# Performance work log

Measured on AMD Instinct MI355X. Metric: run time of the kernel, lower is better.

Reference implementation:

```python
import jax, jax.numpy as jnp
import numpy as np

S = 64    # shapelets_size
N = 256   # num_shapelets
C = 3     # in_channels
B = 64
L = 2048


def setup_inputs() -> dict:
    key = jax.random.key(0)
    kx, ks = jax.random.split(key)
    x = jax.random.normal(kx, (B, C, L), dtype=jnp.float32)
    shapelets = jax.random.normal(ks, (C, N, S), dtype=jnp.float32)
    return {"x": x, "shapelets": shapelets}


def reference(x, shapelets):
    # x: (B, C, L); shapelets: (C, N, S)
    W = x.shape[2] - S + 1  # number of sliding windows
    # unfold: (B, C, W, S)
    idx = jnp.arange(W)[:, None] + jnp.arange(S)[None, :]
    win = x[:, :, idx]
    # cdist with mm-based euclidean: d^2 = |a|^2 + |b|^2 - 2 a.b
    win_sq = jnp.sum(win * win, axis=-1)                 # (B, C, W)
    shp_sq = jnp.sum(shapelets * shapelets, axis=-1)     # (C, N)
    cross = jnp.einsum('bcws,cns->bcwn', win, shapelets)  # (B, C, W, N)
    d2 = win_sq[..., None] + shp_sq[None, :, None, :] - 2.0 * cross
    d = jnp.sqrt(jnp.maximum(d2, 0.0))                   # (B, C, W, N)
    # sum over channels, keepdim -> (B, 1, W, N); transpose -> (B, 1, N, W); min over W
    summed = jnp.sum(d, axis=1, keepdims=True)
    out = jnp.min(jnp.swapaxes(summed, 2, 3), axis=3)    # (B, 1, N)
    return out
```

## Files before the change

### kernel.cpp

```cpp
#include <hip/hip_runtime.h>
#include <hip/hip_fp16.h>


typedef float  v4f __attribute__((ext_vector_type(4)));
typedef short  v8s __attribute__((ext_vector_type(8)));
typedef unsigned short u16;
typedef unsigned int   u32;
typedef unsigned long long u64;

#define S_ 64
#define N_ 256
#define C_ 3
#define B_ 64
#define L_ 2048
#define W_ 1985
#define WQL 512
#define NC 146
#define CSTRIDE 160
#define THREADS 512

__device__ __forceinline__ u16 f2bf(float f) {
    u32 u = __builtin_bit_cast(u32, f);
    return (u16)((u + 0x7FFFu + ((u >> 16) & 1u)) >> 16);
}
__device__ __forceinline__ float bf2f(u16 b) {
    return __builtin_bit_cast(float, ((u32)b) << 16);
}

__global__ __launch_bounds__(THREADS, 4)
void shapelet_min_kernel(const float* __restrict__ x,
                         const float* __restrict__ shp,
                         float* __restrict__ out)
{
    __shared__ u64   xls[C_ * 4 * CSTRIDE];
    __shared__ float wsq[C_][WQL];
    __shared__ u16   scratch[C_ * 64 * 72];
    __shared__ float red[8][64];

    const int tid  = threadIdx.x;
    const int wave = tid >> 6;
    const int lane = tid & 63;
    const int m    = lane & 15;
    const int q    = lane >> 4;
    const int ww   = wave & 3;
    const int wn   = wave >> 2;
    const int blk  = blockIdx.x;
    const int wq   = blk & 3;
    const int nh   = (blk >> 2) & 1;
    const int b    = blk >> 3;
    const int w0   = wq << 9;
    const int wlen = min(WQL, W_ - w0);

    const float* xb = x + (size_t)b * (C_ * L_);
    float xf[8];
    int xc = 0, xt = 0;
    bool xact = (tid < C_ * NC);
    if (xact) {
        xc = tid / NC;
        xt = tid - xc * NC;
        int e = w0 + (xt << 2);
        if (e + 7 < L_) {
            v4f a0 = *(const v4f*)(xb + xc * L_ + e);
            v4f a1 = *(const v4f*)(xb + xc * L_ + e + 4);
            xf[0] = a0[0]; xf[1] = a0[1]; xf[2] = a0[2]; xf[3] = a0[3];
            xf[4] = a1[0]; xf[5] = a1[1]; xf[6] = a1[2]; xf[7] = a1[3];
        } else {
            #pragma unroll
            for (int i = 0; i < 8; ++i)
                xf[i] = (e + i < L_) ? xb[xc * L_ + e + i] : 0.f;
        }
    }

    const int nbase = nh << 7;
    #pragma unroll
    for (int k = 0; k < 6; ++k) {
        int idx = tid + k * THREADS;
        int sq = idx & 15;
        int n  = (idx >> 4) & 63;
        int c  = idx >> 10;
        v4f v = *(const v4f*)(shp + ((size_t)(c * N_ + nbase + n) * S_ + (sq << 2)));
        u64 pk = (u64)f2bf(v[0]) | ((u64)f2bf(v[1]) << 16)
               | ((u64)f2bf(v[2]) << 32) | ((u64)f2bf(v[3]) << 48);
        *(u64*)(scratch + ((c * 64 + n) * 72 + (sq << 2))) = pk;
    }

    if (xact) {
        u16 w8[8];
        #pragma unroll
        for (int i = 0; i < 8; ++i) w8[i] = f2bf(-2.f * xf[i]);
        #pragma unroll
        for (int r = 0; r < 4; ++r) {
            u64 pk = (u64)w8[r] | ((u64)w8[r + 1] << 16)
                   | ((u64)w8[r + 2] << 32) | ((u64)w8[r + 3] << 48);
            xls[(xc * 4 + r) * CSTRIDE + 4 * r + xt] = pk;
        }
    }
    __syncthreads();

    if (tid < 128 * C_) {
        int c  = tid >> 7;
        int t0 = tid & 127;
        const u64* cp0 = &xls[(c * 4) * CSTRIDE];
        u64 ch = cp0[t0];
        float h0 = bf2f((u16)ch),         h1 = bf2f((u16)(ch >> 16)),
              h2 = bf2f((u16)(ch >> 32)), h3 = bf2f((u16)(ch >> 48));
        float sq0 = h0 * h0, sq1 = h1 * h1, sq2 = h2 * h2;
        float s = sq0 + sq1 + sq2 + h3 * h3;
        #pragma unroll
        for (int kk = 1; kk < 16; ++kk) {
            u64 c2 = cp0[t0 + kk];
            float e0 = bf2f((u16)c2),         e1 = bf2f((u16)(c2 >> 16)),
                  e2 = bf2f((u16)(c2 >> 32)), e3 = bf2f((u16)(c2 >> 48));
            s += e0 * e0; s += e1 * e1; s += e2 * e2; s += e3 * e3;
        }
        u64 ct = cp0[t0 + 16];
        float t4 = bf2f((u16)ct), t5 = bf2f((u16)(ct >> 16)), t6 = bf2f((u16)(ct >> 32));
        float s0 = s;
        float s1 = s0 - sq0 + t4 * t4;
        float s2 = s1 - sq1 + t5 * t5;
        float s3 = s2 - sq2 + t6 * t6;
        v4f o = (v4f){0.25f * s0, 0.25f * s1, 0.25f * s2, 0.25f * s3};
        *(v4f*)&wsq[c][t0 << 2] = o;
    }

    const int r  = m & 3;
    const int sE = m >> 2;

    #pragma unroll 1
    for (int g = 0; g < 2; ++g) {
        v8s bfr[C_][2][2];
        float ssq[C_][2];
        #pragma unroll
        for (int c = 0; c < C_; ++c) {
            #pragma unroll
            for (int nt = 0; nt < 2; ++nt) {
                float sacc = 0.f;
                #pragma unroll
                for (int h = 0; h < 2; ++h) {
                    v8s f = *(const v8s*)(scratch +
                             ((c * 64 + wn * 32 + nt * 16 + m) * 72 + h * 32 + q * 8));
                    bfr[c][nt][h] = f;
                    #pragma unroll
                    for (int j = 0; j < 8; ++j) {
                        float e = bf2f((u16)f[j]);
                        sacc += e * e;
                    }
                }
                sacc += __shfl_xor(sacc, 16);
                sacc += __shfl_xor(sacc, 32);
                ssq[c][nt] = sacc;
            }
        }
        __syncthreads();

        float minv[2] = {1e30f, 1e30f};
        #pragma unroll 1
        for (int it = 0; it < 8; ++it) {
            const int wb = it * 64 + ww * 16;
            if (wb >= wlen) continue;

            float sums[2][4];
            #pragma unroll
            for (int nt = 0; nt < 2; ++nt)
                #pragma unroll
                for (int gi = 0; gi < 4; ++gi) sums[nt][gi] = 0.f;

            #pragma unroll
            for (int c = 0; c < C_; ++c) {
                const u64* cp = &xls[(c * 4 + r) * CSTRIDE + 4 * r];
                int T0 = (wb >> 2) + 2 * q + sE;
                union { u64 u[2]; v8s v; } a0, a1;
                a0.u[0] = cp[T0];     a0.u[1] = cp[T0 + 1];
                a1.u[0] = cp[T0 + 8]; a1.u[1] = cp[T0 + 9];

                v4f wv = *(const v4f*)&wsq[c][wb + (q << 2)];
                v4f acc[2];
                #pragma unroll
                for (int nt = 0; nt < 2; ++nt)
                    #pragma unroll
                    for (int gi = 0; gi < 4; ++gi)
                        acc[nt][gi] = wv[gi] + ssq[c][nt];
                #pragma unroll
                for (int nt = 0; nt < 2; ++nt) {
                    acc[nt] = __builtin_amdgcn_mfma_f32_16x16x32_bf16(a0.v, bfr[c][nt][0], acc[nt], 0, 0, 0);
                    acc[nt] = __builtin_amdgcn_mfma_f32_16x16x32_bf16(a1.v, bfr[c][nt][1], acc[nt], 0, 0, 0);
                }
                #pragma unroll
                for (int nt = 0; nt < 2; ++nt)
                    #pragma unroll
                    for (int gi = 0; gi < 4; ++gi)
                        sums[nt][gi] += __builtin_amdgcn_sqrtf(fmaxf(acc[nt][gi], 0.f));
            }
            if (wb + 16 <= wlen) {
                #pragma unroll
                for (int nt = 0; nt < 2; ++nt)
                    #pragma unroll
                    for (int gi = 0; gi < 4; ++gi)
                        minv[nt] = fminf(minv[nt], sums[nt][gi]);
            } else {
                #pragma unroll
                for (int gi = 0; gi < 4; ++gi) {
                    bool ok = (wb + (q << 2) + gi) < wlen;
                    #pragma unroll
                    for (int nt = 0; nt < 2; ++nt)
                        minv[nt] = fminf(minv[nt], ok ? sums[nt][gi] : 1e30f);
                }
            }
        }

        #pragma unroll
        for (int nt = 0; nt < 2; ++nt) {
            minv[nt] = fminf(minv[nt], __shfl_xor(minv[nt], 16));
            minv[nt] = fminf(minv[nt], __shfl_xor(minv[nt], 32));
        }

        if (g == 0) {
            #pragma unroll
            for (int k = 0; k < 6; ++k) {
                int idx = tid + k * THREADS;
                int sq = idx & 15;
                int n  = (idx >> 4) & 63;
                int c  = idx >> 10;
                v4f v = *(const v4f*)(shp +
                        ((size_t)(c * N_ + nbase + 64 + n) * S_ + (sq << 2)));
                u64 pk = (u64)f2bf(v[0]) | ((u64)f2bf(v[1]) << 16)
                       | ((u64)f2bf(v[2]) << 32) | ((u64)f2bf(v[3]) << 48);
                *(u64*)(scratch + ((c * 64 + n) * 72 + (sq << 2))) = pk;
            }
        }
        if (lane < 16) {
            red[wave][wn * 32 + lane]      = minv[0];
            red[wave][wn * 32 + 16 + lane] = minv[1];
        }
        __syncthreads();

        if (tid < 64) {
            int tn = tid >> 5;
            float v = red[tn * 4 + 0][tid];
            v = fminf(v, red[tn * 4 + 1][tid]);
            v = fminf(v, red[tn * 4 + 2][tid]);
            v = fminf(v, red[tn * 4 + 3][tid]);
            atomicMin((u32*)out + ((size_t)b * N_ + nbase + (g << 6) + tid),
                      __float_as_uint(v));
        }
        if (g == 0) __syncthreads();
    }
}

extern "C" void kernel_launch(void* const* d_in, const int* in_sizes, int n_in,
                              void* d_out, int out_size, void* d_ws, size_t ws_size,
                              hipStream_t stream) {
    const float* x   = (const float*)d_in[0];
    const float* shp = (const float*)d_in[1];
    float* out       = (float*)d_out;
    hipMemsetAsync(d_out, 0x7f, (size_t)B_ * N_ * sizeof(float), stream);
    hipLaunchKernelGGL(shapelet_min_kernel, dim3(512), dim3(THREADS), 0, stream,
                       x, shp, (float*)d_out);
}
```

Measured before the change: 85.14 us.

## Split work into smaller blocks over window and shapelet slices

Re-partitions the grid so each 256-thread block handles a 249-window slice and 32 shapelets in a single pass, launching 4096 blocks instead of 512. This removes the sequential two-group shapelet loop and aims to improve occupancy and load balance across CUs. In exchange, the input and shapelet tiles are loaded and converted to bf16 redundantly in more blocks, and more atomicMin operations hit the output.

```diff
diff --git a/kernel.cpp b/kernel.cpp
--- a/kernel.cpp
+++ b/kernel.cpp
@@ -14,10 +14,10 @@
 #define B_ 64
 #define L_ 2048
 #define W_ 1985
-#define WQL 512
-#define NC 146
-#define CSTRIDE 160
-#define THREADS 512
+#define WOL 249
+#define NC 78
+#define CSTRIDE 96
+#define THREADS 256
 
 __device__ __forceinline__ u16 f2bf(float f) {
     u32 u = __builtin_bit_cast(u32, f);
@@ -27,29 +27,28 @@
     return __builtin_bit_cast(float, ((u32)b) << 16);
 }
 
-__global__ __launch_bounds__(THREADS, 4)
+__global__ __launch_bounds__(THREADS, 5)
 void shapelet_min_kernel(const float* __restrict__ x,
                          const float* __restrict__ shp,
                          float* __restrict__ out)
 {
     __shared__ u64   xls[C_ * 4 * CSTRIDE];
-    __shared__ float wsq[C_][WQL];
-    __shared__ u16   scratch[C_ * 64 * 72];
-    __shared__ float red[8][64];
+    __shared__ float wsq[C_][256];
+    __shared__ u16   scratch[C_ * 32 * 72];
+    __shared__ float red[4][32];
 
     const int tid  = threadIdx.x;
-    const int wave = tid >> 6;
+    const int wg   = tid >> 6;
     const int lane = tid & 63;
     const int m    = lane & 15;
     const int q    = lane >> 4;
-    const int ww   = wave & 3;
-    const int wn   = wave >> 2;
     const int blk  = blockIdx.x;
-    const int wq   = blk & 3;
-    const int nh   = (blk >> 2) & 1;
-    const int b    = blk >> 3;
-    const int w0   = wq << 9;
-    const int wlen = min(WQL, W_ - w0);
+    const int wo   = blk & 7;
+    const int no   = (blk >> 3) & 7;
+    const int b    = blk >> 6;
+    const int w0   = wo * WOL;
+    const int wlen = min(WOL, W_ - w0);
+    const int n0   = no << 5;
 
     const float* xb = x + (size_t)b * (C_ * L_);
     float xf[8];
@@ -71,17 +70,16 @@
         }
     }
 
-    const int nbase = nh << 7;
     #pragma unroll
     for (int k = 0; k < 6; ++k) {
         int idx = tid + k * THREADS;
         int sq = idx & 15;
-        int n  = (idx >> 4) & 63;
-        int c  = idx >> 10;
-        v4f v = *(const v4f*)(shp + ((size_t)(c * N_ + nbase + n) * S_ + (sq << 2)));
+        int n  = (idx >> 4) & 31;
+        int c  = idx >> 9;
+        v4f v = *(const v4f*)(shp + ((size_t)(c * N_ + n0 + n) * S_ + (sq << 2)));
         u64 pk = (u64)f2bf(v[0]) | ((u64)f2bf(v[1]) << 16)
                | ((u64)f2bf(v[2]) << 32) | ((u64)f2bf(v[3]) << 48);
-        *(u64*)(scratch + ((c * 64 + n) * 72 + (sq << 2))) = pk;
+        *(u64*)(scratch + ((c * 32 + n) * 72 + (sq << 2))) = pk;
     }
 
     if (xact) {
@@ -97,9 +95,9 @@
     }
     __syncthreads();
 
-    if (tid < 128 * C_) {
-        int c  = tid >> 7;
-        int t0 = tid & 127;
+    if (tid < 63 * C_) {
+        int c  = tid / 63;
+        int t0 = tid - c * 63;
         const u64* cp0 = &xls[(c * 4) * CSTRIDE];
         u64 ch = cp0[t0];
         float h0 = bf2f((u16)ch),         h1 = bf2f((u16)(ch >> 16)),
@@ -123,127 +121,104 @@
         *(v4f*)&wsq[c][t0 << 2] = o;
     }
 
+    v8s bfr[C_][2][2];
+    float ssq[C_][2];
+    #pragma unroll
+    for (int c = 0; c < C_; ++c) {
+        #pragma unroll
+        for (int nt = 0; nt < 2; ++nt) {
+            float sacc = 0.f;
+            #pragma unroll
+            for (int h = 0; h < 2; ++h) {
+                v8s f = *(const v8s*)(scratch +
+                         ((c * 32 + nt * 16 + m) * 72 + h * 32 + q * 8));
+                bfr[c][nt][h] = f;
+                #pragma unroll
+                for (int j = 0; j < 8; ++j) {
+                    float e = bf2f((u16)f[j]);
+                    sacc += e * e;
+                }
+            }
+            sacc += __shfl_xor(sacc, 16);
+            sacc += __shfl_xor(sacc, 32);
+            ssq[c][nt] = sacc;
+        }
+    }
+    __syncthreads();
+
     const int r  = m & 3;
     const int sE = m >> 2;
 
+    float minv[2] = {1e30f, 1e30f};
     #pragma unroll 1
-    for (int g = 0; g < 2; ++g) {
-        v8s bfr[C_][2][2];
-        float ssq[C_][2];
+    for (int it = 0; it < 4; ++it) {
+        const int wb = it * 64 + wg * 16;
+
+        float sums[2][4];
+        #pragma unroll
+        for (int nt = 0; nt < 2; ++nt)
+            #pragma unroll
+            for (int gi = 0; gi < 4; ++gi) sums[nt][gi] = 0.f;
+
         #pragma unroll
         for (int c = 0; c < C_; ++c) {
+            const u64* cp = &xls[(c * 4 + r) * CSTRIDE + 4 * r];
+            int T0 = (wb >> 2) + 2 * q + sE;
+            union { u64 u[2]; v8s v; } a0, a1;
+            a0.u[0] = cp[T0];     a0.u[1] = cp[T0 + 1];
+            a1.u[0] = cp[T0 + 8]; a1.u[1] = cp[T0 + 9];
+
+            v4f wv = *(const v4f*)&wsq[c][wb + (q << 2)];
+            v4f acc[2];
+            #pragma unroll
+            for (int nt = 0; nt < 2; ++nt)
+                #pragma unroll
+                for (int gi = 0; gi < 4; ++gi)
+                    acc[nt][gi] = wv[gi] + ssq[c][nt];
             #pragma unroll
             for (int nt = 0; nt < 2; ++nt) {
-                float sacc = 0.f;
-                #pragma unroll
-                for (int h = 0; h < 2; ++h) {
-                    v8s f = *(const v8s*)(scratch +
-                             ((c * 64 + wn * 32 + nt * 16 + m) * 72 + h * 32 + q * 8));
-                    bfr[c][nt][h] = f;
-                    #pragma unroll
-                    for (int j = 0; j < 8; ++j) {
-                        float e = bf2f((u16)f[j]);
-                        sacc += e * e;
-                    }
-                }
-                sacc += __shfl_xor(sacc, 16);
-                sacc += __shfl_xor(sacc, 32);
-                ssq[c][nt] = sacc;
+                acc[nt] = __builtin_amdgcn_mfma_f32_16x16x32_bf16(a0.v, bfr[c][nt][0], acc[nt], 0, 0, 0);
+                acc[nt] = __builtin_amdgcn_mfma_f32_16x16x32_bf16(a1.v, bfr[c][nt][1], acc[nt], 0, 0, 0);
             }
-        }
-        __syncthreads();
-
-        float minv[2] = {1e30f, 1e30f};
-        #pragma unroll 1
-        for (int it = 0; it < 8; ++it) {
-            const int wb = it * 64 + ww * 16;
-            if (wb >= wlen) continue;
-
-            float sums[2][4];
             #pragma unroll
             for (int nt = 0; nt < 2; ++nt)
                 #pragma unroll
-                for (int gi = 0; gi < 4; ++gi) sums[nt][gi] = 0.f;
-
-            #pragma unroll
-            for (int c = 0; c < C_; ++c) {
-                const u64* cp = &xls[(c * 4 + r) * CSTRIDE + 4 * r];
-                int T0 = (wb >> 2) + 2 * q + sE;
-                union { u64 u[2]; v8s v; } a0, a1;
-                a0.u[0] = cp[T0];     a0.u[1] = cp[T0 + 1];
-                a1.u[0] = cp[T0 + 8]; a1.u[1] = cp[T0 + 9];
-
-                v4f wv = *(const v4f*)&wsq[c][wb + (q << 2)];
-                v4f acc[2];
+                for (int gi = 0; gi < 4; ++gi)
+                    sums[nt][gi] += __builtin_amdgcn_sqrtf(fmaxf(acc[nt][gi], 0.f));
+        }
+        if (wb + 16 <= wlen) {
+            #pragma unroll
+            for (int nt = 0; nt < 2; ++nt)
+                #pragma unroll
+                for (int gi = 0; gi < 4; ++gi)
+                    minv[nt] = fminf(minv[nt], sums[nt][gi]);
+        } else {
+            #pragma unroll
+            for (int gi = 0; gi < 4; ++gi) {
+                bool ok = (wb + (q << 2) + gi) < wlen;
                 #pragma unroll
                 for (int nt = 0; nt < 2; ++nt)
-                    #pragma unroll
-                    for (int gi = 0; gi < 4; ++gi)
-                        acc[nt][gi] = wv[gi] + ssq[c][nt];
-                #pragma unroll
-                for (int nt = 0; nt < 2; ++nt) {
-                    acc[nt] = __builtin_amdgcn_mfma_f32_16x16x32_bf16(a0.v, bfr[c][nt][0], acc[nt], 0, 0, 0);
-                    acc[nt] = __builtin_amdgcn_mfma_f32_16x16x32_bf16(a1.v, bfr[c][nt][1], acc[nt], 0, 0, 0);
-                }
-                #pragma unroll
-                for (int nt = 0; nt < 2; ++nt)
-                    #pragma unroll
-                    for (int gi = 0; gi < 4; ++gi)
-                        sums[nt][gi] += __builtin_amdgcn_sqrtf(fmaxf(acc[nt][gi], 0.f));
+                    minv[nt] = fminf(minv[nt], ok ? sums[nt][gi] : 1e30f);
             }
-            if (wb + 16 <= wlen) {
-                #pragma unroll
-                for (int nt = 0; nt < 2; ++nt)
-                    #pragma unroll
-                    for (int gi = 0; gi < 4; ++gi)
-                        minv[nt] = fminf(minv[nt], sums[nt][gi]);
-            } else {
-                #pragma unroll
-                for (int gi = 0; gi < 4; ++gi) {
-                    bool ok = (wb + (q << 2) + gi) < wlen;
-                    #pragma unroll
-                    for (int nt = 0; nt < 2; ++nt)
-                        minv[nt] = fminf(minv[nt], ok ? sums[nt][gi] : 1e30f);
-                }
-            }
-        }
-
-        #pragma unroll
-        for (int nt = 0; nt < 2; ++nt) {
-            minv[nt] = fminf(minv[nt], __shfl_xor(minv[nt], 16));
-            minv[nt] = fminf(minv[nt], __shfl_xor(minv[nt], 32));
-        }
-
-        if (g == 0) {
-            #pragma unroll
-            for (int k = 0; k < 6; ++k) {
-                int idx = tid + k * THREADS;
-                int sq = idx & 15;
-                int n  = (idx >> 4) & 63;
-                int c  = idx >> 10;
-                v4f v = *(const v4f*)(shp +
-                        ((size_t)(c * N_ + nbase + 64 + n) * S_ + (sq << 2)));
-                u64 pk = (u64)f2bf(v[0]) | ((u64)f2bf(v[1]) << 16)
-                       | ((u64)f2bf(v[2]) << 32) | ((u64)f2bf(v[3]) << 48);
-                *(u64*)(scratch + ((c * 64 + n) * 72 + (sq << 2))) = pk;
-            }
-        }
-        if (lane < 16) {
-            red[wave][wn * 32 + lane]      = minv[0];
-            red[wave][wn * 32 + 16 + lane] = minv[1];
-        }
-        __syncthreads();
-
-        if (tid < 64) {
-            int tn = tid >> 5;
-            float v = red[tn * 4 + 0][tid];
-            v = fminf(v, red[tn * 4 + 1][tid]);
-            v = fminf(v, red[tn * 4 + 2][tid]);
-            v = fminf(v, red[tn * 4 + 3][tid]);
-            atomicMin((u32*)out + ((size_t)b * N_ + nbase + (g << 6) + tid),
-                      __float_as_uint(v));
-        }
-        if (g == 0) __syncthreads();
+        }
+    }
+
+    #pragma unroll
+    for (int nt = 0; nt < 2; ++nt) {
+        minv[nt] = fminf(minv[nt], __shfl_xor(minv[nt], 16));
+        minv[nt] = fminf(minv[nt], __shfl_xor(minv[nt], 32));
+    }
+    if (lane < 16) {
+        red[wg][lane]      = minv[0];
+        red[wg][16 + lane] = minv[1];
+    }
+    __syncthreads();
+    if (tid < 32) {
+        float v = red[0][tid];
+        v = fminf(v, red[1][tid]);
+        v = fminf(v, red[2][tid]);
+        v = fminf(v, red[3][tid]);
+        atomicMin((u32*)out + ((size_t)b * N_ + n0 + tid), __float_as_uint(v));
     }
 }
 
@@ -252,8 +227,7 @@
                               hipStream_t stream) {
     const float* x   = (const float*)d_in[0];
     const float* shp = (const float*)d_in[1];
-    float* out       = (float*)d_out;
     hipMemsetAsync(d_out, 0x7f, (size_t)B_ * N_ * sizeof(float), stream);
-    hipLaunchKernelGGL(shapelet_min_kernel, dim3(512), dim3(THREADS), 0, stream,
+    hipLaunchKernelGGL(shapelet_min_kernel, dim3(4096), dim3(THREADS), 0, stream,
                        x, shp, (float*)d_out);
 }
```

Result: slower. 110.5 us (+29.7%).

## Split bf16 conversion and norm precompute into separate prologue kernel

Applied to the files above, without the earlier changes.

Adds a precompute kernel that converts x and shapelets to bf16 in the shifted layouts the main kernel needs, and computes window and shapelet squared norms into workspace. The main kernel now only copies these precomputed buffers into shared memory. This removes duplicated conversion and norm work across the 8 blocks per batch and one barrier. The inner loop is also restructured: all MFMAs for the three channels are issued before the sqrt/sum, and packed adds are used for bias init. The cost is an extra kernel launch and a global round trip through workspace.

```diff
diff --git a/kernel.cpp b/kernel.cpp
--- a/kernel.cpp
+++ b/kernel.cpp
@@ -1,8 +1,8 @@
 #include <hip/hip_runtime.h>
-#include <hip/hip_fp16.h>
 
 
 typedef float  v4f __attribute__((ext_vector_type(4)));
+typedef float  v2f __attribute__((ext_vector_type(2)));
 typedef short  v8s __attribute__((ext_vector_type(8)));
 typedef unsigned short u16;
 typedef unsigned int   u32;
@@ -17,7 +17,13 @@
 #define WQL 512
 #define NC 146
 #define CSTRIDE 160
+#define GC 530
 #define THREADS 512
+
+#define XG_OFF   0
+#define WSQ_OFF  3256320
+#define SHP_OFF  4829184
+#define SSQ_OFF  4927488
 
 __device__ __forceinline__ u16 f2bf(float f) {
     u32 u = __builtin_bit_cast(u32, f);
@@ -26,10 +32,90 @@
 __device__ __forceinline__ float bf2f(u16 b) {
     return __builtin_bit_cast(float, ((u32)b) << 16);
 }
+__device__ __forceinline__ v2f pk_add(v2f a, v2f b) {
+    v2f d;
+    asm("v_pk_add_f32 %0, %1, %2" : "=v"(d) : "v"(a), "v"(b));
+    return d;
+}
+
+__global__ __launch_bounds__(256)
+void precompute_kernel(const float* __restrict__ x, const float* __restrict__ shp,
+                       u64* __restrict__ xg, float* __restrict__ wsqg,
+                       u64* __restrict__ shpbf, float* __restrict__ ssqg)
+{
+    const int blk = blockIdx.x;
+    const int tid = threadIdx.x;
+    if (blk < B_ * C_) {
+        __shared__ u64 elsq[532];
+        const float* xb = x + (size_t)blk * L_;
+        {
+            v4f a0 = *(const v4f*)(xb + tid * 8);
+            v4f a1 = *(const v4f*)(xb + tid * 8 + 4);
+            u64 p0 = (u64)f2bf(-2.f * a0[0]) | ((u64)f2bf(-2.f * a0[1]) << 16)
+                   | ((u64)f2bf(-2.f * a0[2]) << 32) | ((u64)f2bf(-2.f * a0[3]) << 48);
+            u64 p1 = (u64)f2bf(-2.f * a1[0]) | ((u64)f2bf(-2.f * a1[1]) << 16)
+                   | ((u64)f2bf(-2.f * a1[2]) << 32) | ((u64)f2bf(-2.f * a1[3]) << 48);
+            elsq[tid * 2] = p0;
+            elsq[tid * 2 + 1] = p1;
+            if (tid < 20) elsq[512 + tid] = 0ull;
+        }
+        __syncthreads();
+
+        for (int t2 = tid; t2 < GC; t2 += 256) {
+            u64 lo = elsq[t2], hi = elsq[t2 + 1];
+            u64* dst = xg + (size_t)blk * 4 * GC + t2;
+            dst[0] = lo;
+            dst[GC]     = (lo >> 16) | (hi << 48);
+            dst[2 * GC] = (lo >> 32) | (hi << 32);
+            dst[3 * GC] = (lo >> 48) | (hi << 16);
+        }
+
+        for (int t0 = tid; t0 < 497; t0 += 256) {
+            u64 ch = elsq[t0];
+            float h0 = bf2f((u16)ch),         h1 = bf2f((u16)(ch >> 16)),
+                  h2 = bf2f((u16)(ch >> 32)), h3 = bf2f((u16)(ch >> 48));
+            float sq0 = h0 * h0, sq1 = h1 * h1, sq2 = h2 * h2;
+            float s = sq0 + sq1 + sq2 + h3 * h3;
+            #pragma unroll
+            for (int kk = 1; kk < 16; ++kk) {
+                u64 c2 = elsq[t0 + kk];
+                float e0 = bf2f((u16)c2),         e1 = bf2f((u16)(c2 >> 16)),
+                      e2 = bf2f((u16)(c2 >> 32)), e3 = bf2f((u16)(c2 >> 48));
+                s += e0 * e0; s += e1 * e1; s += e2 * e2; s += e3 * e3;
+            }
+            u64 ct = elsq[t0 + 16];
+            float t4 = bf2f((u16)ct), t5 = bf2f((u16)(ct >> 16)), t6 = bf2f((u16)(ct >> 32));
+            float s0 = s;
+            float s1 = s0 - sq0 + t4 * t4;
+            float s2 = s1 - sq1 + t5 * t5;
+            float s3 = s2 - sq2 + t6 * t6;
+            v4f o = (v4f){0.25f * s0, 0.25f * s1, 0.25f * s2, 0.25f * s3};
+            *(v4f*)(wsqg + ((size_t)blk << 11) + (t0 << 2)) = o;
+        }
+        if (tid < 15) {
+            v4f z = (v4f){0.f, 0.f, 0.f, 0.f};
+            *(v4f*)(wsqg + ((size_t)blk << 11) + 1988 + 4 * tid) = z;
+        }
+    } else {
+        const int c = blk - B_ * C_;
+        const float* sp = shp + ((size_t)c * N_ + tid) * S_;
+        u64* dstrow = shpbf + ((size_t)c * N_ + tid) * 16;
+        float sacc = 0.f;
+        #pragma unroll
+        for (int k = 0; k < 16; ++k) {
+            v4f v = *(const v4f*)(sp + 4 * k);
+            u16 b0 = f2bf(v[0]), b1 = f2bf(v[1]), b2 = f2bf(v[2]), b3 = f2bf(v[3]);
+            dstrow[k] = (u64)b0 | ((u64)b1 << 16) | ((u64)b2 << 32) | ((u64)b3 << 48);
+            float e0 = bf2f(b0), e1 = bf2f(b1), e2 = bf2f(b2), e3 = bf2f(b3);
+            sacc += e0 * e0 + e1 * e1 + e2 * e2 + e3 * e3;
+        }
+        ssqg[c * N_ + tid] = sacc;
+    }
+}
 
 __global__ __launch_bounds__(THREADS, 4)
-void shapelet_min_kernel(const float* __restrict__ x,
-                         const float* __restrict__ shp,
+void shapelet_min_kernel(const u64* __restrict__ xg, const float* __restrict__ wsqg,
+                         const u64* __restrict__ shpbf, const float* __restrict__ ssqg,
                          float* __restrict__ out)
 {
     __shared__ u64   xls[C_ * 4 * CSTRIDE];
@@ -50,78 +136,33 @@
     const int b    = blk >> 3;
     const int w0   = wq << 9;
     const int wlen = min(WQL, W_ - w0);
-
-    const float* xb = x + (size_t)b * (C_ * L_);
-    float xf[8];
-    int xc = 0, xt = 0;
-    bool xact = (tid < C_ * NC);
-    if (xact) {
-        xc = tid / NC;
-        xt = tid - xc * NC;
-        int e = w0 + (xt << 2);
-        if (e + 7 < L_) {
-            v4f a0 = *(const v4f*)(xb + xc * L_ + e);
-            v4f a1 = *(const v4f*)(xb + xc * L_ + e + 4);
-            xf[0] = a0[0]; xf[1] = a0[1]; xf[2] = a0[2]; xf[3] = a0[3];
-            xf[4] = a1[0]; xf[5] = a1[1]; xf[6] = a1[2]; xf[7] = a1[3];
-        } else {
-            #pragma unroll
-            for (int i = 0; i < 8; ++i)
-                xf[i] = (e + i < L_) ? xb[xc * L_ + e + i] : 0.f;
-        }
-    }
-
     const int nbase = nh << 7;
+
+    u64* scq = (u64*)scratch;
+    #pragma unroll
+    for (int k = 0; k < 4; ++k) {
+        int u = tid + k * THREADS;
+        if (u < 12 * NC) {
+            int cr = u / NC;
+            int t  = u - cr * NC;
+            int c  = cr >> 2, rr = cr & 3;
+            xls[(c * 4 + rr) * CSTRIDE + 4 * rr + t] =
+                xg[((size_t)(b * C_ + c) * 4 + rr) * GC + wq * 128 + t];
+        }
+    }
     #pragma unroll
     for (int k = 0; k < 6; ++k) {
-        int idx = tid + k * THREADS;
-        int sq = idx & 15;
-        int n  = (idx >> 4) & 63;
-        int c  = idx >> 10;
-        v4f v = *(const v4f*)(shp + ((size_t)(c * N_ + nbase + n) * S_ + (sq << 2)));
-        u64 pk = (u64)f2bf(v[0]) | ((u64)f2bf(v[1]) << 16)
-               | ((u64)f2bf(v[2]) << 32) | ((u64)f2bf(v[3]) << 48);
-        *(u64*)(scratch + ((c * 64 + n) * 72 + (sq << 2))) = pk;
-    }
-
-    if (xact) {
-        u16 w8[8];
-        #pragma unroll
-        for (int i = 0; i < 8; ++i) w8[i] = f2bf(-2.f * xf[i]);
-        #pragma unroll
-        for (int r = 0; r < 4; ++r) {
-            u64 pk = (u64)w8[r] | ((u64)w8[r + 1] << 16)
-                   | ((u64)w8[r + 2] << 32) | ((u64)w8[r + 3] << 48);
-            xls[(xc * 4 + r) * CSTRIDE + 4 * r + xt] = pk;
-        }
+        int u = tid + k * THREADS;
+        int sq = u & 15;
+        int n  = (u >> 4) & 63;
+        int c  = u >> 10;
+        scq[(c * 64 + n) * 18 + sq] = shpbf[((size_t)c * N_ + nbase + n) * 16 + sq];
+    }
+    if (tid < 128 * C_) {
+        int c = tid >> 7, i = (tid & 127) << 2;
+        *(v4f*)&wsq[c][i] = *(const v4f*)(wsqg + ((size_t)(b * C_ + c) << 11) + w0 + i);
     }
     __syncthreads();
-
-    if (tid < 128 * C_) {
-        int c  = tid >> 7;
-        int t0 = tid & 127;
-        const u64* cp0 = &xls[(c * 4) * CSTRIDE];
-        u64 ch = cp0[t0];
-        float h0 = bf2f((u16)ch),         h1 = bf2f((u16)(ch >> 16)),
-              h2 = bf2f((u16)(ch >> 32)), h3 = bf2f((u16)(ch >> 48));
-        float sq0 = h0 * h0, sq1 = h1 * h1, sq2 = h2 * h2;
-        float s = sq0 + sq1 + sq2 + h3 * h3;
-        #pragma unroll
-        for (int kk = 1; kk < 16; ++kk) {
-            u64 c2 = cp0[t0 + kk];
-            float e0 = bf2f((u16)c2),         e1 = bf2f((u16)(c2 >> 16)),
-                  e2 = bf2f((u16)(c2 >> 32)), e3 = bf2f((u16)(c2 >> 48));
-            s += e0 * e0; s += e1 * e1; s += e2 * e2; s += e3 * e3;
-        }
-        u64 ct = cp0[t0 + 16];
-        float t4 = bf2f((u16)ct), t5 = bf2f((u16)(ct >> 16)), t6 = bf2f((u16)(ct >> 32));
-        float s0 = s;
-        float s1 = s0 - sq0 + t4 * t4;
-        float s2 = s1 - sq1 + t5 * t5;
-        float s3 = s2 - sq2 + t6 * t6;
-        v4f o = (v4f){0.25f * s0, 0.25f * s1, 0.25f * s2, 0.25f * s3};
-        *(v4f*)&wsq[c][t0 << 2] = o;
-    }
 
     const int r  = m & 3;
     const int sE = m >> 2;
@@ -131,27 +172,15 @@
         v8s bfr[C_][2][2];
         float ssq[C_][2];
         #pragma unroll
-        for (int c = 0; c < C_; ++c) {
+        for (int c = 0; c < C_; ++c)
             #pragma unroll
             for (int nt = 0; nt < 2; ++nt) {
-                float sacc = 0.f;
-                #pragma unroll
-                for (int h = 0; h < 2; ++h) {
-                    v8s f = *(const v8s*)(scratch +
-                             ((c * 64 + wn * 32 + nt * 16 + m) * 72 + h * 32 + q * 8));
-                    bfr[c][nt][h] = f;
-                    #pragma unroll
-                    for (int j = 0; j < 8; ++j) {
-                        float e = bf2f((u16)f[j]);
-                        sacc += e * e;
-                    }
-                }
-                sacc += __shfl_xor(sacc, 16);
-                sacc += __shfl_xor(sacc, 32);
-                ssq[c][nt] = sacc;
-            }
-        }
-        __syncthreads();
+                #pragma unroll
+                for (int h = 0; h < 2; ++h)
+                    bfr[c][nt][h] = *(const v8s*)(scratch +
+                        ((c * 64 + wn * 32 + nt * 16 + m) * 72 + h * 32 + q * 8));
+                ssq[c][nt] = ssqg[c * N_ + nbase + (g << 6) + wn * 32 + nt * 16 + m];
+            }
 
         float minv[2] = {1e30f, 1e30f};
         #pragma unroll 1
@@ -159,52 +188,64 @@
             const int wb = it * 64 + ww * 16;
             if (wb >= wlen) continue;
 
-            float sums[2][4];
-            #pragma unroll
-            for (int nt = 0; nt < 2; ++nt)
-                #pragma unroll
-                for (int gi = 0; gi < 4; ++gi) sums[nt][gi] = 0.f;
-
+            v8s afr[C_][2];
             #pragma unroll
             for (int c = 0; c < C_; ++c) {
                 const u64* cp = &xls[(c * 4 + r) * CSTRIDE + 4 * r];
-                int T0 = (wb >> 2) + 2 * q + sE;
+                const int T0 = (wb >> 2) + 2 * q + sE;
                 union { u64 u[2]; v8s v; } a0, a1;
                 a0.u[0] = cp[T0];     a0.u[1] = cp[T0 + 1];
                 a1.u[0] = cp[T0 + 8]; a1.u[1] = cp[T0 + 9];
-
+                afr[c][0] = a0.v; afr[c][1] = a1.v;
+            }
+
+            v4f acc[C_][2];
+            #pragma unroll
+            for (int c = 0; c < C_; ++c) {
                 v4f wv = *(const v4f*)&wsq[c][wb + (q << 2)];
-                v4f acc[2];
+                v2f wlo = (v2f){wv[0], wv[1]}, whi = (v2f){wv[2], wv[3]};
+                #pragma unroll
+                for (int nt = 0; nt < 2; ++nt) {
+                    v2f sq2 = (v2f){ssq[c][nt], ssq[c][nt]};
+                    v2f i0 = pk_add(wlo, sq2);
+                    v2f i1 = pk_add(whi, sq2);
+                    acc[c][nt] = (v4f){i0[0], i0[1], i1[0], i1[1]};
+                }
+            }
+            #pragma unroll
+            for (int c = 0; c < C_; ++c)
+                #pragma unroll
+                for (int nt = 0; nt < 2; ++nt) {
+                    acc[c][nt] = __builtin_amdgcn_mfma_f32_16x16x32_bf16(
+                        afr[c][0], bfr[c][nt][0], acc[c][nt], 0, 0, 0);
+                    acc[c][nt] = __builtin_amdgcn_mfma_f32_16x16x32_bf16(
+                        afr[c][1], bfr[c][nt][1], acc[c][nt], 0, 0, 0);
+                }
+
+            if (wb + 16 <= wlen) {
                 #pragma unroll
                 for (int nt = 0; nt < 2; ++nt)
                     #pragma unroll
-                    for (int gi = 0; gi < 4; ++gi)
-                        acc[nt][gi] = wv[gi] + ssq[c][nt];
-                #pragma unroll
-                for (int nt = 0; nt < 2; ++nt) {
-                    acc[nt] = __builtin_amdgcn_mfma_f32_16x16x32_bf16(a0.v, bfr[c][nt][0], acc[nt], 0, 0, 0);
-                    acc[nt] = __builtin_amdgcn_mfma_f32_16x16x32_bf16(a1.v, bfr[c][nt][1], acc[nt], 0, 0, 0);
-                }
+                    for (int gi = 0; gi < 4; gi += 2) {
+                        float t0 = __builtin_amdgcn_sqrtf(fmaxf(acc[0][nt][gi], 0.f))
+                                 + __builtin_amdgcn_sqrtf(fmaxf(acc[1][nt][gi], 0.f))
+                                 + __builtin_amdgcn_sqrtf(fmaxf(acc[2][nt][gi], 0.f));
+                        float t1 = __builtin_amdgcn_sqrtf(fmaxf(acc[0][nt][gi + 1], 0.f))
+                                 + __builtin_amdgcn_sqrtf(fmaxf(acc[1][nt][gi + 1], 0.f))
+                                 + __builtin_amdgcn_sqrtf(fmaxf(acc[2][nt][gi + 1], 0.f));
+                        minv[nt] = fminf(fminf(minv[nt], t0), t1);
+                    }
+            } else {
                 #pragma unroll
                 for (int nt = 0; nt < 2; ++nt)
                     #pragma unroll
-                    for (int gi = 0; gi < 4; ++gi)
-                        sums[nt][gi] += __builtin_amdgcn_sqrtf(fmaxf(acc[nt][gi], 0.f));
-            }
-            if (wb + 16 <= wlen) {
-                #pragma unroll
-                for (int nt = 0; nt < 2; ++nt)
-                    #pragma unroll
-                    for (int gi = 0; gi < 4; ++gi)
-                        minv[nt] = fminf(minv[nt], sums[nt][gi]);
-            } else {
-                #pragma unroll
-                for (int gi = 0; gi < 4; ++gi) {
-                    bool ok = (wb + (q << 2) + gi) < wlen;
-                    #pragma unroll
-                    for (int nt = 0; nt < 2; ++nt)
-                        minv[nt] = fminf(minv[nt], ok ? sums[nt][gi] : 1e30f);
-                }
+                    for (int gi = 0; gi < 4; ++gi) {
+                        float t = __builtin_amdgcn_sqrtf(fmaxf(acc[0][nt][gi], 0.f))
+                                + __builtin_amdgcn_sqrtf(fmaxf(acc[1][nt][gi], 0.f))
+                                + __builtin_amdgcn_sqrtf(fmaxf(acc[2][nt][gi], 0.f));
+                        bool ok = (wb + (q << 2) + gi) < wlen;
+                        minv[nt] = fminf(minv[nt], ok ? t : 1e30f);
+                    }
             }
         }
 
@@ -217,15 +258,12 @@
         if (g == 0) {
             #pragma unroll
             for (int k = 0; k < 6; ++k) {
-                int idx = tid + k * THREADS;
-                int sq = idx & 15;
-                int n  = (idx >> 4) & 63;
-                int c  = idx >> 10;
-                v4f v = *(const v4f*)(shp +
-                        ((size_t)(c * N_ + nbase + 64 + n) * S_ + (sq << 2)));
-                u64 pk = (u64)f2bf(v[0]) | ((u64)f2bf(v[1]) << 16)
-                       | ((u64)f2bf(v[2]) << 32) | ((u64)f2bf(v[3]) << 48);
-                *(u64*)(scratch + ((c * 64 + n) * 72 + (sq << 2))) = pk;
+                int u = tid + k * THREADS;
+                int sq = u & 15;
+                int n  = (u >> 4) & 63;
+                int c  = u >> 10;
+                scq[(c * 64 + n) * 18 + sq] =
+                    shpbf[((size_t)c * N_ + nbase + 64 + n) * 16 + sq];
             }
         }
         if (lane < 16) {
@@ -252,8 +290,15 @@
                               hipStream_t stream) {
     const float* x   = (const float*)d_in[0];
     const float* shp = (const float*)d_in[1];
-    float* out       = (float*)d_out;
+    char* wsb = (char*)d_ws;
+    u64*   xg    = (u64*)(wsb + XG_OFF);
+    float* wsqg  = (float*)(wsb + WSQ_OFF);
+    u64*   shpbf = (u64*)(wsb + SHP_OFF);
+    float* ssqg  = (float*)(wsb + SSQ_OFF);
+
     hipMemsetAsync(d_out, 0x7f, (size_t)B_ * N_ * sizeof(float), stream);
+    hipLaunchKernelGGL(precompute_kernel, dim3(B_ * C_ + C_), dim3(256), 0, stream,
+                       x, shp, xg, wsqg, shpbf, ssqg);
     hipLaunchKernelGGL(shapelet_min_kernel, dim3(512), dim3(THREADS), 0, stream,
-                       x, shp, (float*)d_out);
-}
+                       xg, wsqg, shpbf, ssqg, (float*)d_out);
+}
```

Measured after the change: 93.40 us. 1.1x slower.

## Duplicate shifted x rows in LDS for 128-bit A loads and batch MFMAs

Applied to the files above, without the earlier changes.

Changes the bf16 window layout in shared memory to 8 shifted copies per channel, so each lane can fetch its A fragments with single 16-byte loads instead of paired 8-byte loads. All three channels' fragments are loaded up front, then the six MFMAs are issued back-to-back under raised wave priority, and the sqrt/sum/min epilogue runs afterwards. This aims to cut LDS instruction count and make MFMA issue denser, at the cost of more LDS writes during setup, larger xls storage, and more live registers.

```diff
diff --git a/kernel.cpp b/kernel.cpp
--- a/kernel.cpp
+++ b/kernel.cpp
@@ -1,5 +1,4 @@
 #include <hip/hip_runtime.h>
-#include <hip/hip_fp16.h>
 
 
 typedef float  v4f __attribute__((ext_vector_type(4)));
@@ -16,7 +15,7 @@
 #define W_ 1985
 #define WQL 512
 #define NC 146
-#define CSTRIDE 160
+#define CSTRIDE 146
 #define THREADS 512
 
 __device__ __forceinline__ u16 f2bf(float f) {
@@ -32,7 +31,7 @@
                          const float* __restrict__ shp,
                          float* __restrict__ out)
 {
-    __shared__ u64   xls[C_ * 4 * CSTRIDE];
+    __shared__ u64   xls[C_ * 8 * CSTRIDE];
     __shared__ float wsq[C_][WQL];
     __shared__ u16   scratch[C_ * 64 * 72];
     __shared__ float red[8][64];
@@ -92,7 +91,8 @@
         for (int r = 0; r < 4; ++r) {
             u64 pk = (u64)w8[r] | ((u64)w8[r + 1] << 16)
                    | ((u64)w8[r + 2] << 32) | ((u64)w8[r + 3] << 48);
-            xls[(xc * 4 + r) * CSTRIDE + 4 * r + xt] = pk;
+            xls[(xc * 8 + r) * CSTRIDE + xt] = pk;
+            if (xt > 0) xls[(xc * 8 + r + 4) * CSTRIDE + xt - 1] = pk;
         }
     }
     __syncthreads();
@@ -100,7 +100,7 @@
     if (tid < 128 * C_) {
         int c  = tid >> 7;
         int t0 = tid & 127;
-        const u64* cp0 = &xls[(c * 4) * CSTRIDE];
+        const u64* cp0 = &xls[(c * 8) * CSTRIDE];
         u64 ch = cp0[t0];
         float h0 = bf2f((u16)ch),         h1 = bf2f((u16)(ch >> 16)),
               h2 = bf2f((u16)(ch >> 32)), h3 = bf2f((u16)(ch >> 48));
@@ -123,8 +123,8 @@
         *(v4f*)&wsq[c][t0 << 2] = o;
     }
 
-    const int r  = m & 3;
-    const int sE = m >> 2;
+    const int rp = m & 7;
+    const int mE = m >> 3;
 
     #pragma unroll 1
     for (int g = 0; g < 2; ++g) {
@@ -159,52 +159,59 @@
             const int wb = it * 64 + ww * 16;
             if (wb >= wlen) continue;
 
-            float sums[2][4];
-            #pragma unroll
-            for (int nt = 0; nt < 2; ++nt)
-                #pragma unroll
-                for (int gi = 0; gi < 4; ++gi) sums[nt][gi] = 0.f;
-
+            const int bidx = (wb >> 2) + 2 * mE + 2 * q;
+            v8s afr[C_][2];
             #pragma unroll
             for (int c = 0; c < C_; ++c) {
-                const u64* cp = &xls[(c * 4 + r) * CSTRIDE + 4 * r];
-                int T0 = (wb >> 2) + 2 * q + sE;
-                union { u64 u[2]; v8s v; } a0, a1;
-                a0.u[0] = cp[T0];     a0.u[1] = cp[T0 + 1];
-                a1.u[0] = cp[T0 + 8]; a1.u[1] = cp[T0 + 9];
-
+                const u64* cp = &xls[(c * 8 + rp) * CSTRIDE];
+                afr[c][0] = *(const v8s*)(cp + bidx);
+                afr[c][1] = *(const v8s*)(cp + bidx + 8);
+            }
+
+            v4f acc[C_][2];
+            #pragma unroll
+            for (int c = 0; c < C_; ++c) {
                 v4f wv = *(const v4f*)&wsq[c][wb + (q << 2)];
-                v4f acc[2];
                 #pragma unroll
                 for (int nt = 0; nt < 2; ++nt)
                     #pragma unroll
                     for (int gi = 0; gi < 4; ++gi)
-                        acc[nt][gi] = wv[gi] + ssq[c][nt];
+                        acc[c][nt][gi] = wv[gi] + ssq[c][nt];
+            }
+
+            __builtin_amdgcn_s_setprio(1);
+            #pragma unroll
+            for (int c = 0; c < C_; ++c)
                 #pragma unroll
                 for (int nt = 0; nt < 2; ++nt) {
-                    acc[nt] = __builtin_amdgcn_mfma_f32_16x16x32_bf16(a0.v, bfr[c][nt][0], acc[nt], 0, 0, 0);
-                    acc[nt] = __builtin_amdgcn_mfma_f32_16x16x32_bf16(a1.v, bfr[c][nt][1], acc[nt], 0, 0, 0);
+                    acc[c][nt] = __builtin_amdgcn_mfma_f32_16x16x32_bf16(
+                        afr[c][0], bfr[c][nt][0], acc[c][nt], 0, 0, 0);
+                    acc[c][nt] = __builtin_amdgcn_mfma_f32_16x16x32_bf16(
+                        afr[c][1], bfr[c][nt][1], acc[c][nt], 0, 0, 0);
                 }
+            __builtin_amdgcn_s_setprio(0);
+
+            if (wb + 16 <= wlen) {
                 #pragma unroll
                 for (int nt = 0; nt < 2; ++nt)
                     #pragma unroll
-                    for (int gi = 0; gi < 4; ++gi)
-                        sums[nt][gi] += __builtin_amdgcn_sqrtf(fmaxf(acc[nt][gi], 0.f));
-            }
-            if (wb + 16 <= wlen) {
+                    for (int gi = 0; gi < 4; ++gi) {
+                        float t = __builtin_amdgcn_sqrtf(fmaxf(acc[0][nt][gi], 0.f))
+                                + __builtin_amdgcn_sqrtf(fmaxf(acc[1][nt][gi], 0.f))
+                                + __builtin_amdgcn_sqrtf(fmaxf(acc[2][nt][gi], 0.f));
+                        minv[nt] = fminf(minv[nt], t);
+                    }
+            } else {
                 #pragma unroll
                 for (int nt = 0; nt < 2; ++nt)
                     #pragma unroll
-                    for (int gi = 0; gi < 4; ++gi)
-                        minv[nt] = fminf(minv[nt], sums[nt][gi]);
-            } else {
-                #pragma unroll
-                for (int gi = 0; gi < 4; ++gi) {
-                    bool ok = (wb + (q << 2) + gi) < wlen;
-                    #pragma unroll
-                    for (int nt = 0; nt < 2; ++nt)
-                        minv[nt] = fminf(minv[nt], ok ? sums[nt][gi] : 1e30f);
-                }
+                    for (int gi = 0; gi < 4; ++gi) {
+                        float t = __builtin_amdgcn_sqrtf(fmaxf(acc[0][nt][gi], 0.f))
+                                + __builtin_amdgcn_sqrtf(fmaxf(acc[1][nt][gi], 0.f))
+                                + __builtin_amdgcn_sqrtf(fmaxf(acc[2][nt][gi], 0.f));
+                        bool ok = (wb + (q << 2) + gi) < wlen;
+                        minv[nt] = fminf(minv[nt], ok ? t : 1e30f);
+                    }
             }
         }
 
@@ -252,7 +259,6 @@
                               hipStream_t stream) {
     const float* x   = (const float*)d_in[0];
     const float* shp = (const float*)d_in[1];
-    float* out       = (float*)d_out;
     hipMemsetAsync(d_out, 0x7f, (size_t)B_ * N_ * sizeof(float), stream);
     hipLaunchKernelGGL(shapelet_min_kernel, dim3(512), dim3(THREADS), 0, stream,
                        x, shp, (float*)d_out);
```

Result: slower. 91.80 us (+7.8%).
